# Optimization experiments

Measured on AMD Instinct MI355X. Metric: run time of the kernel, lower is better.

The kernel has to match this reference:

```python
import jax, jax.numpy as jnp
import numpy as np

# Dimensions derived from LaneATTHead defaults (see shape_source)
B, CIN, CF, FH, FW = 8, 256, 64, 22, 40
A, S = 2784, 72          # n_anchors, n_offsets
NC = 2                   # num_category
D = CF * FH              # per-anchor feature dim = 1408
P = NC + 2 + 2 * S       # proposal dim = 148


def setup_inputs() -> dict:
    key = jax.random.key(0)
    ks = jax.random.split(key, 12)
    sc = 0.02
    return {
        "x": jax.random.normal(ks[0], (B, CIN, FH, FW), jnp.float32),
        "conv_w": jax.random.normal(ks[1], (CF, CIN), jnp.float32) * sc,
        "conv_b": jax.random.normal(ks[2], (CF,), jnp.float32) * sc,
        "attn_w": jax.random.normal(ks[3], (D, A - 1), jnp.float32) * sc,
        "attn_b": jax.random.normal(ks[4], (A - 1,), jnp.float32) * sc,
        "cls_w": jax.random.normal(ks[5], (2 * D, NC), jnp.float32) * sc,
        "cls_b": jax.random.normal(ks[6], (NC,), jnp.float32) * sc,
        "reg_w": jax.random.normal(ks[7], (2 * D, 2 * S), jnp.float32) * sc,
        "reg_b": jax.random.normal(ks[8], (2 * S,), jnp.float32) * sc,
        "anchors": jax.random.uniform(ks[9], (A, P), jnp.float32),
        "cut_xs": jax.random.randint(ks[10], (A, FH), 0, FW, jnp.int32),
        "invalid_mask": jax.random.randint(ks[11], (A, FH), 0, 2, jnp.int32).astype(jnp.bool_),
    }


def reference(x, conv_w, conv_b, attn_w, attn_b, cls_w, cls_b, reg_w, reg_b,
              anchors, cut_xs, invalid_mask):
    # 1x1 conv: [B,CIN,FH,FW] -> [B,CF,FH,FW]
    feats = jnp.einsum('bchw,oc->bohw', x, conv_w) + conv_b[None, :, None, None]

    # cut_anchor_features: gather per-anchor column per row, zero invalid
    rows = jnp.arange(FH)
    g = feats[:, :, rows[None, :], cut_xs]             # [B, CF, A, FH]
    g = jnp.transpose(g, (0, 2, 1, 3))                  # [B, A, CF, FH]
    g = jnp.where(invalid_mask[None, :, None, :], jnp.float32(0), g)
    baf = g.reshape(B, A, D)                            # [B, A, D]

    # attention over other anchors (softmax over A-1 slots)
    scores = baf @ attn_w + attn_b                      # [B, A, A-1]
    attention = jax.nn.softmax(scores, axis=-1)

    # scatter into [A,A] with zero diagonal (row-major off-diag fill, as in eye()+nonzero())
    i = jnp.arange(A)[:, None]
    k = jnp.arange(A - 1)[None, :]
    cols = k + (k >= i).astype(jnp.int32)               # [A, A-1]
    attn_mat = jnp.zeros((B, A, A), baf.dtype).at[:, i, cols].set(attention)

    # weighted pooling (equiv. of the transposed bmm chain)
    att_feat = jnp.einsum('bij,bjd->bid', attn_mat, baf)  # [B, A, D]

    f2 = jnp.concatenate([att_feat, baf], axis=-1)      # [B, A, 2D]
    cls = f2 @ cls_w + cls_b                            # [B, A, NC]
    reg = f2 @ reg_w + reg_b                            # [B, A, 2S]
    reg = jnp.concatenate([reg[..., :S], jax.nn.sigmoid(reg[..., S:])], axis=-1)

    base = jnp.broadcast_to(anchors, (B, A, P))
    # reg_proposals: [:, :, :NC]=cls ; [:, :, NC:NC+2]=anchor ; [:, :, NC+2:]+=reg
    props = jnp.concatenate([cls, base[..., NC:NC + 2], base[..., NC + 2:] + reg], axis=-1)
    return props, attn_mat
```

## Files before the change

kernel.cpp:

```cpp
#include <hip/hip_runtime.h>
#include <stdint.h>

typedef __attribute__((ext_vector_type(8))) __bf16 bf16x8;
typedef __attribute__((ext_vector_type(4))) float f32x4;
typedef __attribute__((ext_vector_type(2))) long long2v;
typedef unsigned short u16;
typedef unsigned char u8;

#define DEV static __device__ __forceinline__

constexpr int NB = 8;
constexpr int AA = 2784;
constexpr int AM1 = 2783;
constexpr int DD = 1408;
constexpr int MT = NB * AA;
constexpr int KP = 2816;

DEV u16 f2bf(float f) {
  uint32_t u = __builtin_bit_cast(uint32_t, f);
  u += 0x7FFFu + ((u >> 16) & 1u);
  return (u16)(u >> 16);
}
DEV float bf2f(unsigned v) { return __builtin_bit_cast(float, v << 16); }
DEV u8 f2f8(float f) {
  return (u8)(__builtin_amdgcn_cvt_pk_fp8_f32(f, f, 0, false) & 0xff);
}
DEV float4 cv4(unsigned w) {
  float4 r;
  r.x = __builtin_amdgcn_cvt_f32_fp8((int)w, 0);
  r.y = __builtin_amdgcn_cvt_f32_fp8((int)w, 1);
  r.z = __builtin_amdgcn_cvt_f32_fp8((int)w, 2);
  r.w = __builtin_amdgcn_cvt_f32_fp8((int)w, 3);
  return r;
}
DEV unsigned pk4(float a, float b, float c, float d) {
  int r = __builtin_amdgcn_cvt_pk_fp8_f32(a, b, 0, false);
  r = __builtin_amdgcn_cvt_pk_fp8_f32(c, d, r, true);
  return (unsigned)r;
}

DEV void load16_lds(const void* g, void* l) {
  auto gp = (const __attribute__((address_space(1))) uint32_t*)(uintptr_t)g;
  auto lp = (__attribute__((address_space(3))) uint32_t*)(uint32_t)(uintptr_t)l;
  __builtin_amdgcn_global_load_lds(gp, lp, 16, 0, 0);
}

#define VMW(n) asm volatile("s_waitcnt vmcnt(" #n ")" ::: "memory")
#define VMW0 asm volatile("s_waitcnt vmcnt(0)" ::: "memory")
#define LGW0 asm volatile("s_waitcnt lgkmcnt(0)" ::: "memory")
#define BARR asm volatile("s_barrier" ::: "memory")
#define SCHB __builtin_amdgcn_sched_barrier(0)

DEV void mf32(f32x4 (&acc)[8][2], const long (&a)[8][2], const long (&b)[2][2]) {
  __builtin_amdgcn_s_setprio(1);
#pragma unroll
  for (int mt = 0; mt < 8; ++mt)
#pragma unroll
    for (int nt = 0; nt < 2; ++nt)
#pragma unroll
      for (int ks = 0; ks < 2; ++ks)
        acc[mt][nt] = __builtin_amdgcn_mfma_f32_16x16x32_fp8_fp8(
            a[mt][ks], b[nt][ks], acc[mt][nt], 0, 0, 0);
  __builtin_amdgcn_s_setprio(0);
}

template <int MODE>
__global__ __launch_bounds__(512) void gemm_k(const u8* __restrict__ A,
                                              const u8* __restrict__ Bt,
                                              u8* __restrict__ out8,
                                              u16* __restrict__ outh,
                                              const float* __restrict__ b1) {
  constexpr int K   = (MODE == 1) ? 1408 : KP;
  constexpr int NT  = K / 128;
  constexpr int LDA = (MODE == 1) ? 1408 : KP;
  constexpr int LDB = (MODE == 1) ? 1408 : KP;
  constexpr int MR  = (MODE == 1) ? MT : AA;
  __shared__ __align__(16) u8 As8[3][32768];
  __shared__ __align__(16) u8 Bs8[3][16384];
  const int tid = threadIdx.x;
  const int lane = tid & 63;
  const int w = tid >> 6;
  const int wr = w >> 2, wc = w & 3;
  const int l16 = lane & 15, lq = lane >> 4;
  const int l7 = l16 & 7;

  const int gx = gridDim.x, gy = gridDim.y;
  const int nwg = gx * gy;
  const int i = blockIdx.x + blockIdx.y * gx;
  const int xcd = i & 7, pos = i >> 3;
  const int q = nwg >> 3, r = nwg & 7;
  const int lid = (xcd < r ? xcd * (q + 1) : r * (q + 1) + (xcd - r) * q) + pos;
  const int m0 = (lid / gy) * 256, n0 = (lid % gy) * 128;

  const u8* Ab = A;
  const u8* Bb = Bt;
  u16* outp = outh;
  if constexpr (MODE == 2) {
    const int bz = blockIdx.z;
    Ab += (size_t)bz * AA * KP;
    Bb += (size_t)bz * DD * KP;
    outp += (size_t)bz * AA * DD;
  }

  auto stA = [&](int buf, int kt) {
#pragma unroll
    for (int inst = 0; inst < 4; ++inst) {
      int c = tid + inst * 512;
      int row = c >> 3, sl = c & 7;
      int sr = m0 + row;
      sr = sr < MR - 1 ? sr : MR - 1;
      load16_lds(Ab + (size_t)sr * LDA + kt * 128 + ((sl ^ (row & 7)) << 4),
                 &As8[buf][c << 4]);
    }
  };
  auto stB = [&](int buf, int kt) {
#pragma unroll
    for (int inst = 0; inst < 2; ++inst) {
      int c = tid + inst * 512;
      int row = c >> 3, sl = c & 7;
      int sr = n0 + row;
      load16_lds(Bb + (size_t)sr * LDB + kt * 128 + ((sl ^ (row & 7)) << 4),
                 &Bs8[buf][c << 4]);
    }
  };
  auto rdA = [&](int buf, int kh, long (&a)[8][2]) {
    const int u = (kh * 4 + lq) ^ l7;
#pragma unroll
    for (int mt = 0; mt < 8; ++mt) {
      int rloc = wr * 128 + mt * 16 + l16;
      long2v v = *(const long2v*)&As8[buf][rloc * 128 + u * 16];
      a[mt][0] = v[0]; a[mt][1] = v[1];
    }
  };
  auto rdB = [&](int buf, int kh, long (&b)[2][2]) {
    const int u = (kh * 4 + lq) ^ l7;
#pragma unroll
    for (int nt = 0; nt < 2; ++nt) {
      int R = wc * 32 + nt * 16 + l16;
      long2v v = *(const long2v*)&Bs8[buf][R * 128 + u * 16];
      b[nt][0] = v[0]; b[nt][1] = v[1];
    }
  };

  f32x4 acc[8][2];
#pragma unroll
  for (int i2 = 0; i2 < 8; ++i2)
#pragma unroll
    for (int j = 0; j < 2; ++j) acc[i2][j] = 0.f;

  long a[8][2], b[2][2];

  stA(0, 0); stB(0, 0);
  stA(1, 1); stB(1, 1);
  VMW(6);
  BARR;

  for (int t = 0; t < NT; ++t) {
    const int c = t % 3, s = (t + 2) % 3;
    if (t + 2 < NT) { stA(s, t + 2); stB(s, t + 2); }
    rdA(c, 0, a); rdB(c, 0, b);
    LGW0; SCHB;
    mf32(acc, a, b);
    rdA(c, 1, a); rdB(c, 1, b);
    LGW0; SCHB;
    mf32(acc, a, b);
    if (t + 2 < NT) VMW(6); else if (t + 1 < NT) VMW0;
    if (t + 1 < NT) BARR;
  }

  if constexpr (MODE == 1) {
#pragma unroll
    for (int mi = 0; mi < 8; ++mi)
#pragma unroll
      for (int r2 = 0; r2 < 4; ++r2) {
        int m = m0 + wr * 128 + mi * 16 + lq * 4 + r2;
        int ii = m % AA;
#pragma unroll
        for (int ni = 0; ni < 2; ++ni) {
          int n = n0 + wc * 32 + ni * 16 + l16;
          if (n >= AM1) continue;
          int col = n + (n >= ii);
          out8[(size_t)m * KP + col] = f2f8(acc[mi][ni][r2] + b1[n]);
        }
      }
  } else {
#pragma unroll
    for (int mi = 0; mi < 8; ++mi)
#pragma unroll
      for (int r2 = 0; r2 < 4; ++r2) {
        int m = m0 + wr * 128 + mi * 16 + lq * 4 + r2;
        if (m >= AA) continue;
        size_t base = (size_t)m * DD;
#pragma unroll
        for (int ni = 0; ni < 2; ++ni) {
          int n = n0 + wc * 32 + ni * 16 + l16;
          outp[base + n] = f2bf(acc[mi][ni][r2] * 0.00390625f);
        }
      }
  }
}

__global__ __launch_bounds__(256) void conv_k(const float* __restrict__ x,
                                              const float* __restrict__ w,
                                              const float* __restrict__ bias,
                                              float* __restrict__ feats) {
  __shared__ float xs[256 * 40];
  int bb = blockIdx.x / 22, h = blockIdx.x % 22;
  const float* xp = x + (size_t)bb * 256 * 880 + h * 40;
  for (int l = threadIdx.x; l < 256 * 40; l += 256)
    xs[l] = xp[(l / 40) * 880 + (l % 40)];
  __syncthreads();
  for (int l = threadIdx.x; l < 64 * 40; l += 256) {
    int o = l / 40, ww = l % 40;
    float acc = bias[o];
    const float* wr = w + o * 256;
#pragma unroll 8
    for (int c = 0; c < 256; ++c) acc += xs[c * 40 + ww] * wr[c];
    feats[((size_t)(bb * 64 + o) * 22 + h) * 40 + ww] = acc;
  }
}

__global__ __launch_bounds__(256) void gt_k(const float* __restrict__ feats,
                                            const int* __restrict__ cut,
                                            const u8* __restrict__ inv,
                                            u16* __restrict__ baf,
                                            u8* __restrict__ baf8,
                                            u8* __restrict__ bft8) {
  unsigned probe = 0;
#pragma unroll
  for (int t = 0; t < 10; ++t)
    probe |= (unsigned)inv[4 * t + 1] | (unsigned)inv[4 * t + 2] | (unsigned)inv[4 * t + 3];
  const bool is_u8 = (probe != 0);
  __shared__ u8 t8[64][65];
  int a0 = blockIdx.x * 64, d0 = blockIdx.y * 64, b = blockIdx.z;
  int tx = threadIdx.x & 63, ty = threadIdx.x >> 6;
  int d = d0 + tx, o = d / 22, h = d - o * 22;
  for (int r = ty; r < 64; r += 4) {
    int a = a0 + r;
    u8 f8 = 0;
    if (a < AA) {
      int msk = is_u8 ? (int)inv[a * 22 + h] : ((const int*)inv)[a * 22 + h];
      float v = 0.f;
      if (!msk) v = feats[((size_t)(b * 64 + o) * 22 + h) * 40 + cut[a * 22 + h]];
      baf[((size_t)b * AA + a) * DD + d] = f2bf(v);
      f8 = f2f8(v);
      baf8[((size_t)b * AA + a) * DD + d] = f8;
    }
    t8[r][tx] = f8;
  }
  __syncthreads();
  for (int r = ty; r < 64; r += 4) {
    int a = a0 + tx;
    if (a < AA) bft8[((size_t)b * DD + d0 + r) * KP + a] = t8[tx][r];
  }
}

__global__ __launch_bounds__(256) void tr_attw_k(const float* __restrict__ w,
                                                 u8* __restrict__ wt8) {
  __shared__ u8 t8[64][65];
  int n0 = blockIdx.x * 64, k0 = blockIdx.y * 64;
  int tx = threadIdx.x & 63, ty = threadIdx.x >> 6;
  for (int r = ty; r < 64; r += 4) {
    int n = n0 + tx;
    t8[r][tx] = (n < AM1) ? f2f8(w[(size_t)(k0 + r) * AM1 + n]) : (u8)0;
  }
  __syncthreads();
  for (int r = ty; r < 64; r += 4)
    wt8[(size_t)(n0 + r) * 1408 + k0 + tx] = t8[tx][r];
}

__global__ __launch_bounds__(256) void wt_k(const float* __restrict__ cw,
                                            const float* __restrict__ rw,
                                            u16* __restrict__ wt) {
  int n = blockIdx.x;
  for (int k = threadIdx.x; k < 2816; k += 256) {
    float v = 0.f;
    if (n < 2) v = cw[(size_t)k * 2 + n];
    else if (n < 146) v = rw[(size_t)k * 144 + (n - 2)];
    wt[(size_t)n * 2816 + k] = f2bf(v);
  }
}

__global__ __launch_bounds__(256) void softf_k(u8* __restrict__ attP) {
  const int row = blockIdx.x;
  const int i = row % AA;
  u8* p = attP + (size_t)row * KP;
  const int t = threadIdx.x;
  const bool act = (t < 176);
  uint4 qw = act ? ((const uint4*)p)[t] : make_uint4(0, 0, 0, 0);
  float v[16];
  { float4 f = cv4(qw.x); v[0] = f.x; v[1] = f.y; v[2] = f.z; v[3] = f.w; }
  { float4 f = cv4(qw.y); v[4] = f.x; v[5] = f.y; v[6] = f.z; v[7] = f.w; }
  { float4 f = cv4(qw.z); v[8] = f.x; v[9] = f.y; v[10] = f.z; v[11] = f.w; }
  { float4 f = cv4(qw.w); v[12] = f.x; v[13] = f.y; v[14] = f.z; v[15] = f.w; }
  const int base = t * 16;
  float mx = -3e38f;
#pragma unroll
  for (int e = 0; e < 16; ++e) {
    int j = base + e;
    if (act && j < AA && j != i) mx = fmaxf(mx, v[e]);
  }
#pragma unroll
  for (int o = 1; o < 64; o <<= 1) mx = fmaxf(mx, __shfl_xor(mx, o));
  __shared__ float rm[4], rs[4];
  if (!(t & 63)) rm[t >> 6] = mx;
  __syncthreads();
  mx = fmaxf(fmaxf(rm[0], rm[1]), fmaxf(rm[2], rm[3]));
  float s = 0.f, ev[16];
#pragma unroll
  for (int e = 0; e < 16; ++e) {
    int j = base + e;
    float tv = (act && j < AA && j != i) ? __expf(v[e] - mx) : 0.f;
    ev[e] = tv; s += tv;
  }
#pragma unroll
  for (int o = 1; o < 64; o <<= 1) s += __shfl_xor(s, o);
  if (!(t & 63)) rs[t >> 6] = s;
  __syncthreads();
  s = (rs[0] + rs[1]) + (rs[2] + rs[3]);
  const float inv = 256.f / s;
#pragma unroll
  for (int e = 0; e < 16; ++e) ev[e] *= inv;
  if (act) {
    uint4 ow;
    ow.x = pk4(ev[0], ev[1], ev[2], ev[3]);
    ow.y = pk4(ev[4], ev[5], ev[6], ev[7]);
    ow.z = pk4(ev[8], ev[9], ev[10], ev[11]);
    ow.w = pk4(ev[12], ev[13], ev[14], ev[15]);
    ((uint4*)p)[t] = ow;
  }
}

__global__ __launch_bounds__(256) void exp_k(const u8* __restrict__ src,
                                             float* __restrict__ dst) {
  int row = blockIdx.x;
  int t = threadIdx.x;
  if (t >= 174) return;
  uint4 qw = ((const uint4*)(src + (size_t)row * KP))[t];
  const float is = 0.00390625f;
  float4 f0 = cv4(qw.x), f1 = cv4(qw.y), f2 = cv4(qw.z), f3 = cv4(qw.w);
  float4* dp = (float4*)(dst + (size_t)row * AA + t * 16);
  dp[0] = make_float4(f0.x * is, f0.y * is, f0.z * is, f0.w * is);
  dp[1] = make_float4(f1.x * is, f1.y * is, f1.z * is, f1.w * is);
  dp[2] = make_float4(f2.x * is, f2.y * is, f2.z * is, f2.w * is);
  dp[3] = make_float4(f3.x * is, f3.y * is, f3.z * is, f3.w * is);
}

__global__ __launch_bounds__(256) void head_k(const u16* __restrict__ A1,
                                              const u16* __restrict__ A2,
                                              const u16* __restrict__ Bt,
                                              float* __restrict__ outf,
                                              const float* __restrict__ b1,
                                              const float* __restrict__ b2,
                                              const float* __restrict__ anch) {
  constexpr int K = 2816, NT = K / 32, BN = 160, HN = 80, NF = 5;
  __shared__ __align__(16) u16 As[2][128 * 32];
  __shared__ __align__(16) u16 Bs[2][BN * 32 + 512];
  const int tid = threadIdx.x;
  const int lane = tid & 63;
  const int wm = tid >> 7, wn = (tid >> 6) & 1;
  const int m0 = blockIdx.x * 128;
  const int l16 = lane & 15, lq = lane >> 4;

  auto stage = [&](int buf, int t) {
    const int k0 = t * 32;
    const u16* Asrc = (k0 < 1408) ? A1 : A2;
    const int kk = (k0 < 1408) ? k0 : k0 - 1408;
#pragma unroll
    for (int inst = 0; inst < 2; ++inst) {
      int c = tid + inst * 256;
      load16_lds(Asrc + (size_t)(m0 + (c >> 2)) * 1408 + kk + (c & 3) * 8, &As[buf][c * 8]);
    }
#pragma unroll
    for (int inst = 0; inst < 3; ++inst) {
      int c = tid + inst * 256;
      int ce = c < BN * 4 ? c : BN * 4 - 1;
      load16_lds(Bt + (size_t)(ce >> 2) * K + k0 + (ce & 3) * 8, &Bs[buf][ce * 8]);
    }
  };

  f32x4 acc[4][NF];
#pragma unroll
  for (int i = 0; i < 4; ++i)
#pragma unroll
    for (int j = 0; j < NF; ++j) acc[i][j] = 0.f;

  stage(0, 0);
  stage(1, 1);
  for (int t = 0; t < NT; ++t) {
    if (t + 1 < NT) VMW(5); else VMW0;
    BARR;
    const int cur = t & 1;
    bf16x8 av[4], bv[NF];
#pragma unroll
    for (int mt = 0; mt < 4; ++mt)
      av[mt] = *(const bf16x8*)&As[cur][(wm * 64 + mt * 16 + l16) * 32 + lq * 8];
#pragma unroll
    for (int nt = 0; nt < NF; ++nt)
      bv[nt] = *(const bf16x8*)&Bs[cur][(wn * HN + nt * 16 + l16) * 32 + lq * 8];
#pragma unroll
    for (int mt = 0; mt < 4; ++mt)
#pragma unroll
      for (int nt = 0; nt < NF; ++nt)
        acc[mt][nt] = __builtin_amdgcn_mfma_f32_16x16x32_bf16(av[mt], bv[nt], acc[mt][nt], 0, 0, 0);
    BARR;
    if (t + 2 < NT) stage(cur, t + 2);
  }

#pragma unroll
  for (int nt = 0; nt < NF; ++nt) {
    int n = wn * HN + nt * 16 + l16;
    if (n >= 146) continue;
#pragma unroll
    for (int mt = 0; mt < 4; ++mt)
#pragma unroll
      for (int r = 0; r < 4; ++r) {
        int m = m0 + wm * 64 + mt * 16 + lq * 4 + r;
        int ii = m % AA;
        float v = acc[mt][nt][r];
        if (n < 2) {
          outf[(size_t)m * 148 + n] = v + b1[n];
          if (n == 0) {
            outf[(size_t)m * 148 + 2] = anch[ii * 148 + 2];
            outf[(size_t)m * 148 + 3] = anch[ii * 148 + 3];
          }
        } else {
          int rr = n - 2;
          v += b2[rr];
          if (rr >= 72) v = 1.f / (1.f + __expf(-v));
          outf[(size_t)m * 148 + 4 + rr] = anch[ii * 148 + 4 + rr] + v;
        }
      }
  }
}

extern "C" void kernel_launch(void* const* d_in, const int* in_sizes, int n_in,
                              void* d_out, int out_size, void* d_ws, size_t ws_size,
                              hipStream_t stream) {
  const float* x       = (const float*)d_in[0];
  const float* conv_w  = (const float*)d_in[1];
  const float* conv_b  = (const float*)d_in[2];
  const float* attn_w  = (const float*)d_in[3];
  const float* attn_b  = (const float*)d_in[4];
  const float* cls_w   = (const float*)d_in[5];
  const float* cls_b   = (const float*)d_in[6];
  const float* reg_w   = (const float*)d_in[7];
  const float* reg_b   = (const float*)d_in[8];
  const float* anchors = (const float*)d_in[9];
  const int*   cut_xs  = (const int*)d_in[10];
  const u8*    inv     = (const u8*)d_in[11];

  float* props = (float*)d_out;
  float* attn  = props + (size_t)MT * 148;
  u16* attf = (u16*)attn;

  char* wp = (char*)d_ws;
  auto take = [&](size_t bytes) { char* p = wp; wp += (bytes + 255) & ~(size_t)255; return p; };
  u16* baf    = (u16*)take((size_t)MT * DD * 2);
  u8*  baf8   = (u8*)take((size_t)MT * DD);
  u8*  baft8  = (u8*)take((size_t)NB * DD * KP);
  u8*  attP8  = (u8*)take((size_t)MT * KP);
  u8*  attwt8 = (u8*)take((size_t)KP * 1408);
  float* feats = (float*)take((size_t)450560 * 4);
  u16* wt      = (u16*)take((size_t)160 * 2816 * 2);

  conv_k<<<dim3(176), 256, 0, stream>>>(x, conv_w, conv_b, feats);
  gt_k<<<dim3(44, 22, 8), 256, 0, stream>>>(feats, cut_xs, inv, baf, baf8, baft8);
  tr_attw_k<<<dim3(44, 22), 256, 0, stream>>>(attn_w, attwt8);
  wt_k<<<dim3(160), 256, 0, stream>>>(cls_w, reg_w, wt);

  gemm_k<1><<<dim3(87, 22), 512, 0, stream>>>(baf8, attwt8, attP8, nullptr, attn_b);
  softf_k<<<dim3(MT), 256, 0, stream>>>(attP8);
  gemm_k<2><<<dim3(11, 11, 8), 512, 0, stream>>>(attP8, baft8, nullptr, attf, nullptr);
  head_k<<<dim3(174), 256, 0, stream>>>(attf, baf, wt, props,
                                        cls_b, reg_b, anchors);
  exp_k<<<dim3(MT), 256, 0, stream>>>(attP8, attn);
}
```

Measured before the change: 707.9 us.

## Widen FP8 GEMM tiles to 256x256 with double-buffered LDS pipeline

The FP8 GEMM kernels now use 256x256 output tiles instead of 256x128, so each wave computes 128x64 and the grids shrink to match. LDS buffering goes from triple to double to fit the larger B tile, and B fragment loads are split so the first MFMA batch can start before all LDS reads finish. The aim is more arithmetic per loaded byte and fewer workgroups. In exchange it raises register pressure with 32 accumulators per wave, shortens the prefetch depth, adds row clamping and bounds guards for the partial N tile, and GEMM2 now wastes some work in that partial tile.

```diff
diff --git a/kernel.cpp b/kernel.cpp
--- a/kernel.cpp
+++ b/kernel.cpp
@@ -47,16 +47,16 @@
 
 #define VMW(n) asm volatile("s_waitcnt vmcnt(" #n ")" ::: "memory")
 #define VMW0 asm volatile("s_waitcnt vmcnt(0)" ::: "memory")
-#define LGW0 asm volatile("s_waitcnt lgkmcnt(0)" ::: "memory")
+#define LGK(n) asm volatile("s_waitcnt lgkmcnt(" #n ")" ::: "memory")
 #define BARR asm volatile("s_barrier" ::: "memory")
 #define SCHB __builtin_amdgcn_sched_barrier(0)
 
-DEV void mf32(f32x4 (&acc)[8][2], const long (&a)[8][2], const long (&b)[2][2]) {
+DEV void mf64(f32x4 (&acc)[8][4], const long (&a)[8][2], const long (&b)[4][2]) {
   __builtin_amdgcn_s_setprio(1);
 #pragma unroll
   for (int mt = 0; mt < 8; ++mt)
 #pragma unroll
-    for (int nt = 0; nt < 2; ++nt)
+    for (int nt = 0; nt < 4; ++nt)
 #pragma unroll
       for (int ks = 0; ks < 2; ++ks)
         acc[mt][nt] = __builtin_amdgcn_mfma_f32_16x16x32_fp8_fp8(
@@ -69,14 +69,15 @@
                                               const u8* __restrict__ Bt,
                                               u8* __restrict__ out8,
                                               u16* __restrict__ outh,
-                                              const float* __restrict__ b1) {
+                                              const float* __restrict__ bias1) {
   constexpr int K   = (MODE == 1) ? 1408 : KP;
   constexpr int NT  = K / 128;
   constexpr int LDA = (MODE == 1) ? 1408 : KP;
   constexpr int LDB = (MODE == 1) ? 1408 : KP;
   constexpr int MR  = (MODE == 1) ? MT : AA;
-  __shared__ __align__(16) u8 As8[3][32768];
-  __shared__ __align__(16) u8 Bs8[3][16384];
+  constexpr int NRB = (MODE == 1) ? KP : 1408;
+  __shared__ __align__(16) u8 As8[2][32768];
+  __shared__ __align__(16) u8 Bs8[2][32768];
   const int tid = threadIdx.x;
   const int lane = tid & 63;
   const int w = tid >> 6;
@@ -90,7 +91,7 @@
   const int xcd = i & 7, pos = i >> 3;
   const int q = nwg >> 3, r = nwg & 7;
   const int lid = (xcd < r ? xcd * (q + 1) : r * (q + 1) + (xcd - r) * q) + pos;
-  const int m0 = (lid / gy) * 256, n0 = (lid % gy) * 128;
+  const int m0 = (lid / gy) * 256, n0 = (lid % gy) * 256;
 
   const u8* Ab = A;
   const u8* Bb = Bt;
@@ -115,10 +116,11 @@
   };
   auto stB = [&](int buf, int kt) {
 #pragma unroll
-    for (int inst = 0; inst < 2; ++inst) {
+    for (int inst = 0; inst < 4; ++inst) {
       int c = tid + inst * 512;
       int row = c >> 3, sl = c & 7;
       int sr = n0 + row;
+      sr = sr < NRB - 1 ? sr : NRB - 1;
       load16_lds(Bb + (size_t)sr * LDB + kt * 128 + ((sl ^ (row & 7)) << 4),
                  &Bs8[buf][c << 4]);
     }
@@ -132,40 +134,39 @@
       a[mt][0] = v[0]; a[mt][1] = v[1];
     }
   };
-  auto rdB = [&](int buf, int kh, long (&b)[2][2]) {
+  auto rdB = [&](int buf, int kh, long (&b)[4][2]) {
     const int u = (kh * 4 + lq) ^ l7;
 #pragma unroll
-    for (int nt = 0; nt < 2; ++nt) {
-      int R = wc * 32 + nt * 16 + l16;
+    for (int nt = 0; nt < 4; ++nt) {
+      int R = wc * 64 + nt * 16 + l16;
       long2v v = *(const long2v*)&Bs8[buf][R * 128 + u * 16];
       b[nt][0] = v[0]; b[nt][1] = v[1];
     }
   };
 
-  f32x4 acc[8][2];
+  f32x4 acc[8][4];
 #pragma unroll
   for (int i2 = 0; i2 < 8; ++i2)
 #pragma unroll
-    for (int j = 0; j < 2; ++j) acc[i2][j] = 0.f;
-
-  long a[8][2], b[2][2];
+    for (int j = 0; j < 4; ++j) acc[i2][j] = 0.f;
+
+  long a[8][2], bA[4][2], bB[4][2];
 
   stA(0, 0); stB(0, 0);
   stA(1, 1); stB(1, 1);
-  VMW(6);
+  VMW(8);
   BARR;
 
   for (int t = 0; t < NT; ++t) {
-    const int c = t % 3, s = (t + 2) % 3;
-    if (t + 2 < NT) { stA(s, t + 2); stB(s, t + 2); }
-    rdA(c, 0, a); rdB(c, 0, b);
-    LGW0; SCHB;
-    mf32(acc, a, b);
-    rdA(c, 1, a); rdB(c, 1, b);
-    LGW0; SCHB;
-    mf32(acc, a, b);
-    if (t + 2 < NT) VMW(6); else if (t + 1 < NT) VMW0;
-    if (t + 1 < NT) BARR;
+    const int cur = t & 1, nxt = cur ^ 1;
+    if (t + 1 < NT) { stA(nxt, t + 1); stB(nxt, t + 1); }
+    rdB(cur, 0, bA); rdA(cur, 0, a); rdB(cur, 1, bB);
+    LGK(4); SCHB;
+    mf64(acc, a, bA);
+    rdA(cur, 1, a);
+    LGK(0); SCHB;
+    mf64(acc, a, bB);
+    if (t + 1 < NT) { VMW0; BARR; }
   }
 
   if constexpr (MODE == 1) {
@@ -176,11 +177,11 @@
         int m = m0 + wr * 128 + mi * 16 + lq * 4 + r2;
         int ii = m % AA;
 #pragma unroll
-        for (int ni = 0; ni < 2; ++ni) {
-          int n = n0 + wc * 32 + ni * 16 + l16;
+        for (int ni = 0; ni < 4; ++ni) {
+          int n = n0 + wc * 64 + ni * 16 + l16;
           if (n >= AM1) continue;
           int col = n + (n >= ii);
-          out8[(size_t)m * KP + col] = f2f8(acc[mi][ni][r2] + b1[n]);
+          out8[(size_t)m * KP + col] = f2f8(acc[mi][ni][r2] + bias1[n]);
         }
       }
   } else {
@@ -192,9 +193,9 @@
         if (m >= AA) continue;
         size_t base = (size_t)m * DD;
 #pragma unroll
-        for (int ni = 0; ni < 2; ++ni) {
-          int n = n0 + wc * 32 + ni * 16 + l16;
-          outp[base + n] = f2bf(acc[mi][ni][r2] * 0.00390625f);
+        for (int ni = 0; ni < 4; ++ni) {
+          int n = n0 + wc * 64 + ni * 16 + l16;
+          if (n < 1408) outp[base + n] = f2bf(acc[mi][ni][r2] * 0.00390625f);
         }
       }
   }
@@ -469,9 +470,9 @@
   tr_attw_k<<<dim3(44, 22), 256, 0, stream>>>(attn_w, attwt8);
   wt_k<<<dim3(160), 256, 0, stream>>>(cls_w, reg_w, wt);
 
-  gemm_k<1><<<dim3(87, 22), 512, 0, stream>>>(baf8, attwt8, attP8, nullptr, attn_b);
+  gemm_k<1><<<dim3(87, 11), 512, 0, stream>>>(baf8, attwt8, attP8, nullptr, attn_b);
   softf_k<<<dim3(MT), 256, 0, stream>>>(attP8);
-  gemm_k<2><<<dim3(11, 11, 8), 512, 0, stream>>>(attP8, baft8, nullptr, attf, nullptr);
+  gemm_k<2><<<dim3(11, 6, 8), 512, 0, stream>>>(attP8, baft8, nullptr, attf, nullptr);
   head_k<<<dim3(174), 256, 0, stream>>>(attf, baf, wt, props,
                                         cls_b, reg_b, anchors);
   exp_k<<<dim3(MT), 256, 0, stream>>>(attP8, attn);
```

After: 727.7 us. +2.8%, slower.

## Shrink GEMM tiles to 128x128 with double buffering for higher occupancy

Applied to the files above, without the earlier changes.

The FP8 GEMM kernels move from a 256x128 tile with triple-buffered LDS to a 128x128 tile with double buffering. This halves per-block LDS and accumulator registers so more blocks fit per CU, with launch bounds raised to request four. The main loop now waits on partial lgkmcnt so the second k-half B fragment loads overlap the first MFMA batch. The cost is less data reuse per tile, twice as many blocks, and a full vmcnt(0) wait each iteration, so there is less prefetch depth. A row clamp is added to the B loads.

```diff
diff --git a/kernel.cpp b/kernel.cpp
--- a/kernel.cpp
+++ b/kernel.cpp
@@ -47,14 +47,14 @@
 
 #define VMW(n) asm volatile("s_waitcnt vmcnt(" #n ")" ::: "memory")
 #define VMW0 asm volatile("s_waitcnt vmcnt(0)" ::: "memory")
-#define LGW0 asm volatile("s_waitcnt lgkmcnt(0)" ::: "memory")
+#define LGK(n) asm volatile("s_waitcnt lgkmcnt(" #n ")" ::: "memory")
 #define BARR asm volatile("s_barrier" ::: "memory")
 #define SCHB __builtin_amdgcn_sched_barrier(0)
 
-DEV void mf32(f32x4 (&acc)[8][2], const long (&a)[8][2], const long (&b)[2][2]) {
+DEV void mf16c(f32x4 (&acc)[4][2], const long (&a)[4][2], const long (&b)[2][2]) {
   __builtin_amdgcn_s_setprio(1);
 #pragma unroll
-  for (int mt = 0; mt < 8; ++mt)
+  for (int mt = 0; mt < 4; ++mt)
 #pragma unroll
     for (int nt = 0; nt < 2; ++nt)
 #pragma unroll
@@ -65,18 +65,19 @@
 }
 
 template <int MODE>
-__global__ __launch_bounds__(512) void gemm_k(const u8* __restrict__ A,
-                                              const u8* __restrict__ Bt,
-                                              u8* __restrict__ out8,
-                                              u16* __restrict__ outh,
-                                              const float* __restrict__ b1) {
+__global__ __launch_bounds__(512, 4) void gemm_k(const u8* __restrict__ A,
+                                                 const u8* __restrict__ Bt,
+                                                 u8* __restrict__ out8,
+                                                 u16* __restrict__ outh,
+                                                 const float* __restrict__ bias1) {
   constexpr int K   = (MODE == 1) ? 1408 : KP;
   constexpr int NT  = K / 128;
   constexpr int LDA = (MODE == 1) ? 1408 : KP;
   constexpr int LDB = (MODE == 1) ? 1408 : KP;
   constexpr int MR  = (MODE == 1) ? MT : AA;
-  __shared__ __align__(16) u8 As8[3][32768];
-  __shared__ __align__(16) u8 Bs8[3][16384];
+  constexpr int NRB = (MODE == 1) ? KP : 1408;
+  __shared__ __align__(16) u8 As8[2][16384];
+  __shared__ __align__(16) u8 Bs8[2][16384];
   const int tid = threadIdx.x;
   const int lane = tid & 63;
   const int w = tid >> 6;
@@ -90,7 +91,7 @@
   const int xcd = i & 7, pos = i >> 3;
   const int q = nwg >> 3, r = nwg & 7;
   const int lid = (xcd < r ? xcd * (q + 1) : r * (q + 1) + (xcd - r) * q) + pos;
-  const int m0 = (lid / gy) * 256, n0 = (lid % gy) * 128;
+  const int m0 = (lid / gy) * 128, n0 = (lid % gy) * 128;
 
   const u8* Ab = A;
   const u8* Bb = Bt;
@@ -104,7 +105,7 @@
 
   auto stA = [&](int buf, int kt) {
 #pragma unroll
-    for (int inst = 0; inst < 4; ++inst) {
+    for (int inst = 0; inst < 2; ++inst) {
       int c = tid + inst * 512;
       int row = c >> 3, sl = c & 7;
       int sr = m0 + row;
@@ -119,15 +120,16 @@
       int c = tid + inst * 512;
       int row = c >> 3, sl = c & 7;
       int sr = n0 + row;
+      sr = sr < NRB - 1 ? sr : NRB - 1;
       load16_lds(Bb + (size_t)sr * LDB + kt * 128 + ((sl ^ (row & 7)) << 4),
                  &Bs8[buf][c << 4]);
     }
   };
-  auto rdA = [&](int buf, int kh, long (&a)[8][2]) {
+  auto rdA = [&](int buf, int kh, long (&a)[4][2]) {
     const int u = (kh * 4 + lq) ^ l7;
 #pragma unroll
-    for (int mt = 0; mt < 8; ++mt) {
-      int rloc = wr * 128 + mt * 16 + l16;
+    for (int mt = 0; mt < 4; ++mt) {
+      int rloc = wr * 64 + mt * 16 + l16;
       long2v v = *(const long2v*)&As8[buf][rloc * 128 + u * 16];
       a[mt][0] = v[0]; a[mt][1] = v[1];
     }
@@ -142,53 +144,52 @@
     }
   };
 
-  f32x4 acc[8][2];
-#pragma unroll
-  for (int i2 = 0; i2 < 8; ++i2)
+  f32x4 acc[4][2];
+#pragma unroll
+  for (int i2 = 0; i2 < 4; ++i2)
 #pragma unroll
     for (int j = 0; j < 2; ++j) acc[i2][j] = 0.f;
 
-  long a[8][2], b[2][2];
+  long a[4][2], bA[2][2], bB[2][2];
 
   stA(0, 0); stB(0, 0);
   stA(1, 1); stB(1, 1);
-  VMW(6);
+  VMW(4);
   BARR;
 
   for (int t = 0; t < NT; ++t) {
-    const int c = t % 3, s = (t + 2) % 3;
-    if (t + 2 < NT) { stA(s, t + 2); stB(s, t + 2); }
-    rdA(c, 0, a); rdB(c, 0, b);
-    LGW0; SCHB;
-    mf32(acc, a, b);
-    rdA(c, 1, a); rdB(c, 1, b);
-    LGW0; SCHB;
-    mf32(acc, a, b);
-    if (t + 2 < NT) VMW(6); else if (t + 1 < NT) VMW0;
-    if (t + 1 < NT) BARR;
+    const int cur = t & 1, nxt = cur ^ 1;
+    if (t + 1 < NT) { stA(nxt, t + 1); stB(nxt, t + 1); }
+    rdB(cur, 0, bA); rdA(cur, 0, a); rdB(cur, 1, bB);
+    LGK(2); SCHB;
+    mf16c(acc, a, bA);
+    rdA(cur, 1, a);
+    LGK(0); SCHB;
+    mf16c(acc, a, bB);
+    if (t + 1 < NT) { VMW0; BARR; }
   }
 
   if constexpr (MODE == 1) {
 #pragma unroll
-    for (int mi = 0; mi < 8; ++mi)
+    for (int mi = 0; mi < 4; ++mi)
 #pragma unroll
       for (int r2 = 0; r2 < 4; ++r2) {
-        int m = m0 + wr * 128 + mi * 16 + lq * 4 + r2;
+        int m = m0 + wr * 64 + mi * 16 + lq * 4 + r2;
         int ii = m % AA;
 #pragma unroll
         for (int ni = 0; ni < 2; ++ni) {
           int n = n0 + wc * 32 + ni * 16 + l16;
           if (n >= AM1) continue;
           int col = n + (n >= ii);
-          out8[(size_t)m * KP + col] = f2f8(acc[mi][ni][r2] + b1[n]);
+          out8[(size_t)m * KP + col] = f2f8(acc[mi][ni][r2] + bias1[n]);
         }
       }
   } else {
 #pragma unroll
-    for (int mi = 0; mi < 8; ++mi)
+    for (int mi = 0; mi < 4; ++mi)
 #pragma unroll
       for (int r2 = 0; r2 < 4; ++r2) {
-        int m = m0 + wr * 128 + mi * 16 + lq * 4 + r2;
+        int m = m0 + wr * 64 + mi * 16 + lq * 4 + r2;
         if (m >= AA) continue;
         size_t base = (size_t)m * DD;
 #pragma unroll
@@ -469,9 +470,9 @@
   tr_attw_k<<<dim3(44, 22), 256, 0, stream>>>(attn_w, attwt8);
   wt_k<<<dim3(160), 256, 0, stream>>>(cls_w, reg_w, wt);
 
-  gemm_k<1><<<dim3(87, 22), 512, 0, stream>>>(baf8, attwt8, attP8, nullptr, attn_b);
+  gemm_k<1><<<dim3(174, 22), 512, 0, stream>>>(baf8, attwt8, attP8, nullptr, attn_b);
   softf_k<<<dim3(MT), 256, 0, stream>>>(attP8);
-  gemm_k<2><<<dim3(11, 11, 8), 512, 0, stream>>>(attP8, baft8, nullptr, attf, nullptr);
+  gemm_k<2><<<dim3(22, 11, 8), 512, 0, stream>>>(attP8, baft8, nullptr, attf, nullptr);
   head_k<<<dim3(174), 256, 0, stream>>>(attf, baf, wt, props,
                                         cls_b, reg_b, anchors);
   exp_k<<<dim3(MT), 256, 0, stream>>>(attP8, attn);
```

Result: faster. 601.8 us (-15.0%).
